# Kernel tuning notes

Hardware: AMD Instinct MI355X
Metric: run time of the kernel (lower is better)

Reference implementation:

```python
import jax, jax.numpy as jnp
import numpy as np

SXY_BF, SC_BF = 70.0, 12.0
COMPAT_BF, COMPAT_SPATIAL = 4.0, 2.0
SXY_SPATIAL = 6
NUM_ITER = 5
N_OUT = 21


def _gkern_depthwise(std, chans):
    # matches gkern(): sig_sq even -> r = sig_sq - 1, s = 2r+1
    sig_sq = std ** 2
    r = sig_sq if sig_sq % 2 else sig_sq - 1
    s = 2 * r + 1
    yy, xx = np.meshgrid(np.arange(s), np.arange(s), indexing='ij')
    k = np.exp(-(((yy - r) ** 2 + (xx - r) ** 2) / (2.0 * sig_sq)))
    k = k / k.sum()
    # original builds a [C,C,s,s] diagonal kernel == depthwise [C,1,s,s]
    return jnp.asarray(np.broadcast_to(k[None, None], (chans, 1, s, s)).copy(), jnp.float32)


def setup_inputs() -> dict:
    key = jax.random.key(0)
    k1, k2 = jax.random.split(key)
    unary = jax.random.uniform(k1, (2, N_OUT, 64, 64), dtype=jnp.float32)
    ref = jax.random.uniform(k2, (2, 3, 64, 64), dtype=jnp.float32) * 255.0  # RGB image
    gk = _gkern_depthwise(SXY_SPATIAL, N_OUT)
    kstd = jnp.asarray([SXY_BF, SXY_BF, SC_BF, SC_BF, SC_BF], jnp.float32)
    return {"unary": unary, "ref": ref, "gk": gk, "kstd": kstd}


def _crf_forward(unary, ref, gk, kstd):
    N, C, H, W = unary.shape
    P = H * W
    # stacked reference features: [y, x, r, g, b]
    yy, xx = jnp.meshgrid(jnp.arange(H, dtype=jnp.float32),
                          jnp.arange(W, dtype=jnp.float32), indexing='ij')
    grid = jnp.broadcast_to(jnp.stack([yy, xx])[None], (N, 2, H, W))
    stacked = jnp.concatenate([grid, ref], axis=1)  # [N,5,H,W]
    feats = (stacked / kstd[None, :, None, None]).reshape(N, -1, P).transpose(0, 2, 1)  # [N,P,5]
    # exact dense Gaussian (bilateral) kernel: K[p,q] = exp(-||f_p - f_q||^2 / 2)
    sq = jnp.sum(feats * feats, axis=-1)  # [N,P]
    d2 = sq[:, :, None] + sq[:, None, :] - 2.0 * jnp.einsum('npd,nqd->npq', feats, feats)
    K = jnp.exp(-0.5 * jnp.maximum(d2, 0.0))  # [N,P,P]

    U = jnp.log(jnp.clip(unary, 1e-5, 1.0))
    q = jax.nn.softmax(U, axis=1)
    pad = gk.shape[-1] // 2
    for i in range(NUM_ITER):
        qbf = jnp.einsum('npq,ncq->ncp', K, q.reshape(N, C, P)).reshape(N, C, H, W)
        qsf = jax.lax.conv_general_dilated(
            q, gk, window_strides=(1, 1), padding=[(pad, pad), (pad, pad)],
            feature_group_count=C, dimension_numbers=('NCHW', 'OIHW', 'NCHW'))
        q_hat = U + COMPAT_BF * qbf + COMPAT_SPATIAL * qsf
        q = jax.nn.softmax(q_hat, axis=1)  # normalize_final_iter=True
    return q


def reference(unary, ref, gk, kstd):
    return _crf_forward(unary, ref, gk, kstd)
```

## Files before the change

### kernel.cpp

```cpp
#include <hip/hip_runtime.h>
#include <math.h>

#ifndef __has_builtin
#define __has_builtin(x) 0
#endif
#if __has_builtin(__builtin_amdgcn_exp2f)
#define EXP2F(x) __builtin_amdgcn_exp2f(x)
#else
#define EXP2F(x) exp2f(x)
#endif

#define L2E  1.44269504088896340736f
#define RL2E 0.69314718055994530942f

#define NBATCH 2
#define NC 21
#define NP 4096
#define KR 35
#define KS 71

typedef _Float16 half_t;
typedef _Float16 h8 __attribute__((ext_vector_type(8)));
typedef _Float16 h4 __attribute__((ext_vector_type(4)));
typedef float f4 __attribute__((ext_vector_type(4)));
#define MFMA16(a, b, c) __builtin_amdgcn_mfma_f32_16x16x32_f16((a), (b), (c), 0, 0, 0)

#define PTILE 128
#define NPT   32
#define SQ    16
#define CHUNK 256
#define STEPS 8
#define NBBIL (NBATCH * NPT * SQ)
#define NBCONV (NBATCH * NC)
#define SEGS_PER_S 1024
#define SEG_HALVES 256

#define OFF_QFEAT 0
#define OFF_QSOA  65536
#define OFF_UT    114688
#define OFF_QSF   311296
#define OFF_G     483328
#define OFF_QH16  485376
#define OFF_PART  845824

#define LDS_BYTES 27648
#define QLS_STRIDE 264

__global__ __launch_bounds__(256) void setup_kernel(
    const float* __restrict__ unary, const float* __restrict__ ref,
    const float* __restrict__ kstd, float* __restrict__ ws,
    float* __restrict__ outq)
{
    int gid = blockIdx.x * 256 + threadIdx.x;
    if (gid < 4096) {
        float s = 0.f;
        for (int t = -KR; t <= KR; ++t) s += expf(-(float)(t * t) * (1.0f / 72.0f));
        int y = gid >> 6, yp = gid & 63;
        int d = y - yp;
        float v = (d >= -KR && d <= KR) ? expf(-(float)(d * d) * (1.0f / 72.0f)) / s : 0.f;
        ((half_t*)(ws + OFF_G))[gid] = (half_t)v;
    }
    if (gid >= NBATCH * NP) return;
    int n = gid >> 12, p = gid & (NP - 1);
    int y = p >> 6, x = p & 63;
    float k0 = kstd[0], k1 = kstd[1], k2 = kstd[2], k3 = kstd[3], k4 = kstd[4];
    const float* rp = ref + n * 3 * NP + p;
    float f0 = (float)y / k0;
    float f1 = (float)x / k1;
    float f2_ = rp[0]      / k2;
    float f3 = rp[NP]     / k3;
    float f4_ = rp[2 * NP] / k4;
    float sq = f0*f0 + f1*f1 + f2_*f2_ + f3*f3 + f4_*f4_;
    float h  = -0.5f * L2E * sq;
    float* qf = ws + OFF_QFEAT + gid * 8;
    qf[0]=L2E*f0; qf[1]=L2E*f1; qf[2]=L2E*f2_; qf[3]=L2E*f3; qf[4]=L2E*f4_;
    qf[5]=h; qf[6]=0.f; qf[7]=0.f;
    float* qs = ws + OFF_QSOA;
    qs[0*8192 + gid] = L2E*f0;  qs[1*8192 + gid] = L2E*f1;
    qs[2*8192 + gid] = L2E*f2_; qs[3*8192 + gid] = L2E*f3;
    qs[4*8192 + gid] = L2E*f4_; qs[5*8192 + gid] = h;

    float U[NC], e[NC];
    const float* up = unary + n * NC * NP + p;
    float m = -1e30f;
    for (int c = 0; c < NC; ++c) {
        float u = up[c * NP];
        u = fminf(fmaxf(u, 1e-5f), 1.0f);
        U[c] = logf(u);
        m = fmaxf(m, U[c]);
    }
    float ssum = 0.f;
    for (int c = 0; c < NC; ++c) { e[c] = EXP2F(L2E * (U[c] - m)); ssum += e[c]; }
    float inv = 1.0f / ssum;
    float* ut = ws + OFF_UT + gid * 24;
    half_t* qh = (half_t*)(ws + OFF_QH16);
    for (int c = 0; c < NC; ++c) {
        float qv = e[c] * inv;
        ut[c] = U[c];
        qh[(n * 24 + c) * NP + p] = (half_t)qv;
        outq[(n * NC + c) * NP + p] = qv;
    }
    ut[21] = 0.f; ut[22] = 0.f; ut[23] = 0.f;
    qh[(n * 24 + 21) * NP + p] = (half_t)0.f;
    qh[(n * 24 + 22) * NP + p] = (half_t)0.f;
    qh[(n * 24 + 23) * NP + p] = (half_t)0.f;
}

__global__ __launch_bounds__(256) void bilat_conv_kernel(
    const float* __restrict__ qfeatA,
    const float* __restrict__ qsoa,
    const half_t* __restrict__ qh16,
    const half_t* __restrict__ gmat,
    half_t* __restrict__ part,
    float* __restrict__ qsf)
{
    __shared__ __align__(16) char lds[LDS_BYTES];
    int b = blockIdx.x;
    int tid = threadIdx.x;
    int l = tid & 63, w = tid >> 6;

    if (b < NBBIL) {
        int n  = b & 1;
        int pt = (b >> 1) & (NPT - 1);
        int s  = b >> 6;
        float*  qsoaS = (float*)lds;
        half_t* qls   = (half_t*)(lds + 6144);

        for (int i = tid; i < 6 * (CHUNK / 4); i += 256) {
            int d = i >> 6, g = i & 63;
            *(f4*)(qsoaS + d * CHUNK + g * 4) =
                *(const f4*)(qsoa + (size_t)d * 8192 + n * NP + s * CHUNK + g * 4);
        }
        for (int i = tid; i < 21 * (CHUNK / 8); i += 256) {
            int c = i >> 5, g = i & 31;
            *(h8*)(qls + c * QLS_STRIDE + g * 8) =
                *(const h8*)(qh16 + (size_t)(n * 24 + c) * NP + s * CHUNK + g * 8);
        }
        for (int i = tid; i < 11 * 33; i += 256) {
            int c = 21 + i / 33, g = i % 33;
            *(h8*)(qls + c * QLS_STRIDE + g * 8) = (h8)(half_t)0.f;
        }
        float pf[2][5], ph[2];
        #pragma unroll
        for (int mt = 0; mt < 2; ++mt) {
            const float* fp = qfeatA + (size_t)(n * NP + pt * PTILE + (w * 2 + mt) * 16 + (l & 15)) * 8;
            #pragma unroll
            for (int i = 0; i < 5; ++i) pf[mt][i] = fp[i] * RL2E;
            ph[mt] = fp[5];
        }
        f4 acc[2][2];
        #pragma unroll
        for (int mt = 0; mt < 2; ++mt) { acc[mt][0] = (f4)0.f; acc[mt][1] = (f4)0.f; }
        int kq = (l >> 4) * 8;
        __syncthreads();

        for (int step = 0; step < STEPS; ++step) {
            int qbase = step * 32 + kq;
            h8 kv[2];
            #pragma unroll
            for (int hf = 0; hf < 2; ++hf) {
                f4 qf0 = *(const f4*)(qsoaS + 0 * CHUNK + qbase + hf * 4);
                f4 qf1 = *(const f4*)(qsoaS + 1 * CHUNK + qbase + hf * 4);
                f4 qf2 = *(const f4*)(qsoaS + 2 * CHUNK + qbase + hf * 4);
                f4 qf3 = *(const f4*)(qsoaS + 3 * CHUNK + qbase + hf * 4);
                f4 qf4 = *(const f4*)(qsoaS + 4 * CHUNK + qbase + hf * 4);
                f4 qf5 = *(const f4*)(qsoaS + 5 * CHUNK + qbase + hf * 4);
                #pragma unroll
                for (int j2 = 0; j2 < 4; ++j2) {
                    float q0 = qf0[j2], q1 = qf1[j2], q2 = qf2[j2];
                    float q3 = qf3[j2], q4 = qf4[j2], qh = qf5[j2];
                    #pragma unroll
                    for (int mt = 0; mt < 2; ++mt) {
                        float e = ph[mt] + qh;
                        e = fmaf(pf[mt][0], q0, e);
                        e = fmaf(pf[mt][1], q1, e);
                        e = fmaf(pf[mt][2], q2, e);
                        e = fmaf(pf[mt][3], q3, e);
                        e = fmaf(pf[mt][4], q4, e);
                        kv[mt][hf * 4 + j2] = (half_t)EXP2F(e);
                    }
                }
            }
            h8 bf0 = *(const h8*)(qls + (size_t)(l & 15) * QLS_STRIDE + qbase);
            h8 bf1 = *(const h8*)(qls + (size_t)(16 + (l & 15)) * QLS_STRIDE + qbase);
            #pragma unroll
            for (int mt = 0; mt < 2; ++mt) {
                acc[mt][0] = MFMA16(kv[mt], bf0, acc[mt][0]);
                acc[mt][1] = MFMA16(kv[mt], bf1, acc[mt][1]);
            }
        }
        #pragma unroll
        for (int mt = 0; mt < 2; ++mt) {
            #pragma unroll
            for (int cht = 0; cht < 2; ++cht) {
                int segFlat = ((((s * 2 + n) * NPT + pt) * 4 + w) * 2 + mt) * 2 + cht;
                h4 hv;
                hv[0] = (half_t)acc[mt][cht][0];
                hv[1] = (half_t)acc[mt][cht][1];
                hv[2] = (half_t)acc[mt][cht][2];
                hv[3] = (half_t)acc[mt][cht][3];
                *(h4*)(part + (size_t)segFlat * SEG_HALVES + l * 4) = hv;
            }
        }
    } else {
        int cb = b - NBBIL;
        int n = cb / NC, c = cb % NC;
        half_t* qt = (half_t*)lds;
        half_t* gl = (half_t*)(lds + 9216);
        half_t* dl = (half_t*)(lds + 18432);

        for (int i = tid; i < 512; i += 256) {
            int row = i >> 3, g = i & 7;
            *(h8*)(gl + row * 72 + g * 8) = *(const h8*)(gmat + row * 64 + g * 8);
        }
        const half_t* qsrc = qh16 + (size_t)(n * 24 + c) * NP;
        for (int i = tid; i < 512; i += 256) {
            int row = i >> 3, g = i & 7;
            h8 v = *(const h8*)(qsrc + row * 64 + g * 8);
            #pragma unroll
            for (int k = 0; k < 8; ++k) qt[(g * 8 + k) * 72 + row] = v[k];
        }
        __syncthreads();

        int m0 = w * 16;
        f4 acc1[4];
        #pragma unroll
        for (int nt = 0; nt < 4; ++nt) acc1[nt] = (f4)0.f;
        #pragma unroll
        for (int ks = 0; ks < 2; ++ks) {
            h8 af = *(const h8*)(gl + (size_t)(m0 + (l & 15)) * 72 + ks * 32 + (l >> 4) * 8);
            #pragma unroll
            for (int nt = 0; nt < 4; ++nt) {
                h8 bf = *(const h8*)(qt + (size_t)(nt * 16 + (l & 15)) * 72 + ks * 32 + (l >> 4) * 8);
                acc1[nt] = MFMA16(af, bf, acc1[nt]);
            }
        }
        #pragma unroll
        for (int nt = 0; nt < 4; ++nt)
            #pragma unroll
            for (int r = 0; r < 4; ++r)
                dl[(size_t)(m0 + (l >> 4) * 4 + r) * 72 + nt * 16 + (l & 15)] = (half_t)acc1[nt][r];
        __syncthreads();

        f4 acc2[4];
        #pragma unroll
        for (int nt = 0; nt < 4; ++nt) acc2[nt] = (f4)0.f;
        #pragma unroll
        for (int ks = 0; ks < 2; ++ks) {
            h8 af = *(const h8*)(dl + (size_t)(m0 + (l & 15)) * 72 + ks * 32 + (l >> 4) * 8);
            #pragma unroll
            for (int nt = 0; nt < 4; ++nt) {
                h8 bf = *(const h8*)(gl + (size_t)(nt * 16 + (l & 15)) * 72 + ks * 32 + (l >> 4) * 8);
                acc2[nt] = MFMA16(af, bf, acc2[nt]);
            }
        }
        float* dst = qsf + (size_t)(n * NC + c) * NP;
        #pragma unroll
        for (int nt = 0; nt < 4; ++nt)
            #pragma unroll
            for (int r = 0; r < 4; ++r)
                dst[(size_t)(m0 + (l >> 4) * 4 + r) * 64 + nt * 16 + (l & 15)] = acc2[nt][r];
    }
}

__global__ __launch_bounds__(256) void reduce_update_kernel(
    const half_t* __restrict__ part, const float* __restrict__ ut_,
    const float* __restrict__ qsf, float* __restrict__ outq,
    half_t* __restrict__ qh16)
{
    __shared__ float red[4096];
    int rb = blockIdx.x;
    int tid = threadIdx.x;
    int n = rb & 1, pt = rb >> 1;

    float acc[16];
    #pragma unroll
    for (int k = 0; k < 16; ++k) acc[k] = 0.f;
    for (int s = 0; s < SQ; ++s) {
        size_t base = (size_t)(((s * 2 + n) * NPT + pt) * 16) * SEG_HALVES;
        #pragma unroll
        for (int k = 0; k < 4; ++k) {
            h4 v = *(const h4*)(part + base + (size_t)(k * 256 + tid) * 4);
            acc[k*4+0] += (float)v[0]; acc[k*4+1] += (float)v[1];
            acc[k*4+2] += (float)v[2]; acc[k*4+3] += (float)v[3];
        }
    }
    #pragma unroll
    for (int k = 0; k < 4; ++k)
        *(f4*)(red + (k * 256 + tid) * 4) =
            (f4){acc[k*4+0], acc[k*4+1], acc[k*4+2], acc[k*4+3]};
    __syncthreads();

    if (tid < PTILE) {
        int pp = tid;
        int p = pt * PTILE + pp;
        int gid = n * NP + p;
        int mt_g = pp >> 4;
        int wv = mt_g >> 1, mtl = mt_g & 1;
        int mrow = pp & 15;
        int lg = mrow >> 2, reg = mrow & 3;
        int segL = wv * 4 + mtl * 2;

        float lg_[NC], e[NC];
        const float* ut = ut_ + (size_t)gid * 24;
        const float* qs = qsf + (size_t)n * NC * NP + p;
        float m = -1e30f;
        #pragma unroll
        for (int c = 0; c < NC; ++c) {
            int cht = c >> 4, chL = c & 15;
            float qb = red[(segL + cht) * 256 + (lg * 16 + chL) * 4 + reg];
            float li = ut[c] + 4.0f * qb + 2.0f * qs[c * NP];
            lg_[c] = li;
            m = fmaxf(m, li);
        }
        float ssum = 0.f;
        #pragma unroll
        for (int c = 0; c < NC; ++c) { e[c] = EXP2F(L2E * (lg_[c] - m)); ssum += e[c]; }
        float inv = 1.0f / ssum;
        #pragma unroll
        for (int c = 0; c < NC; ++c) {
            float qv = e[c] * inv;
            outq[(size_t)(n * NC + c) * NP + p] = qv;
            qh16[(size_t)(n * 24 + c) * NP + p] = (half_t)qv;
        }
    }
}

extern "C" void kernel_launch(void* const* d_in, const int* in_sizes, int n_in,
                              void* d_out, int out_size, void* d_ws, size_t ws_size,
                              hipStream_t stream)
{
    const float* unary = (const float*)d_in[0];
    const float* ref   = (const float*)d_in[1];
    const float* kstd  = (const float*)d_in[3];
    float* ws   = (float*)d_ws;
    float* outq = (float*)d_out;

    const float*  qfeatA = ws + OFF_QFEAT;
    const float*  qsoa   = ws + OFF_QSOA;
    float*        ut     = ws + OFF_UT;
    float*        qsf    = ws + OFF_QSF;
    const half_t* gmat   = (const half_t*)(ws + OFF_G);
    half_t*       qh16   = (half_t*)(ws + OFF_QH16);
    half_t*       part   = (half_t*)(ws + OFF_PART);

    setup_kernel<<<32, 256, 0, stream>>>(unary, ref, kstd, ws, outq);
    for (int it = 0; it < 5; ++it) {
        bilat_conv_kernel<<<NBBIL + NBCONV, 256, 0, stream>>>(
            qfeatA, qsoa, qh16, gmat, part, qsf);
        reduce_update_kernel<<<64, 256, 0, stream>>>(part, ut, qsf, outq, qh16);
    }
}
```

Measured before the change: 159.5 us.

## Precompute dense bilateral kernel once in fp16 and stream it through GEMM

Splits the fused on-the-fly kernel generation and MFMA into a one-time kgen_kernel, which writes the full 2x4096x4096 fp16 Gaussian matrix to workspace in MFMA tile layout. A gemm_conv kernel then reads those tiles each of the five iterations instead of recomputing the exps. The GEMM tile grows to 256 rows per block, and the reduce kernel is resized to match. This removes repeated exp work in exchange for streaming about 64 MB of K per iteration from HBM or cache, and it needs a much larger workspace.

```diff
diff --git a/kernel.cpp b/kernel.cpp
--- a/kernel.cpp
+++ b/kernel.cpp
@@ -25,15 +25,23 @@
 typedef float f4 __attribute__((ext_vector_type(4)));
 #define MFMA16(a, b, c) __builtin_amdgcn_mfma_f32_16x16x32_f16((a), (b), (c), 0, 0, 0)
 
-#define PTILE 128
-#define NPT   32
-#define SQ    16
-#define CHUNK 256
-#define STEPS 8
-#define NBBIL (NBATCH * NPT * SQ)
+#define KG_PTILE 128
+#define KG_NPT   32
+#define KG_SQ    16
+#define KG_CHUNK 256
+#define KG_STEPS 8
+#define NBKG (NBATCH * KG_NPT * KG_SQ)
+
+#define GM_PTILE 256
+#define GM_NPT   16
+#define GM_SQ    16
+#define GM_SLICE 256
+#define GM_STEPS 8
+#define NBGM (NBATCH * GM_NPT * GM_SQ)
 #define NBCONV (NBATCH * NC)
-#define SEGS_PER_S 1024
+
 #define SEG_HALVES 256
+#define PART_PER_NPT 8192
 
 #define OFF_QFEAT 0
 #define OFF_QSOA  65536
@@ -42,6 +50,7 @@
 #define OFF_G     483328
 #define OFF_QH16  485376
 #define OFF_PART  845824
+#define OFF_KF    2942976
 
 #define LDS_BYTES 27648
 #define QLS_STRIDE 264
@@ -106,9 +115,74 @@
     qh[(n * 24 + 23) * NP + p] = (half_t)0.f;
 }
 
-__global__ __launch_bounds__(256) void bilat_conv_kernel(
+__global__ __launch_bounds__(256) void kgen_kernel(
     const float* __restrict__ qfeatA,
     const float* __restrict__ qsoa,
+    half_t* __restrict__ kf)
+{
+    __shared__ __align__(16) float qsoaS[6 * KG_CHUNK];
+    int b = blockIdx.x;
+    int tid = threadIdx.x;
+    int l = tid & 63, w = tid >> 6;
+    int n  = b & 1;
+    int pt = (b >> 1) & (KG_NPT - 1);
+    int s  = b >> 6;
+
+    for (int i = tid; i < 6 * (KG_CHUNK / 4); i += 256) {
+        int d = i >> 6, g = i & 63;
+        *(f4*)(qsoaS + d * KG_CHUNK + g * 4) =
+            *(const f4*)(qsoa + (size_t)d * 8192 + n * NP + s * KG_CHUNK + g * 4);
+    }
+    float pf[2][5], ph[2];
+    #pragma unroll
+    for (int mt = 0; mt < 2; ++mt) {
+        const float* fp = qfeatA + (size_t)(n * NP + pt * KG_PTILE + (w * 2 + mt) * 16 + (l & 15)) * 8;
+        #pragma unroll
+        for (int i = 0; i < 5; ++i) pf[mt][i] = fp[i] * RL2E;
+        ph[mt] = fp[5];
+    }
+    int kq = (l >> 4) * 8;
+    __syncthreads();
+
+    for (int step = 0; step < KG_STEPS; ++step) {
+        int qbase = step * 32 + kq;
+        h8 kv[2];
+        #pragma unroll
+        for (int hf = 0; hf < 2; ++hf) {
+            f4 qf0 = *(const f4*)(qsoaS + 0 * KG_CHUNK + qbase + hf * 4);
+            f4 qf1 = *(const f4*)(qsoaS + 1 * KG_CHUNK + qbase + hf * 4);
+            f4 qf2 = *(const f4*)(qsoaS + 2 * KG_CHUNK + qbase + hf * 4);
+            f4 qf3 = *(const f4*)(qsoaS + 3 * KG_CHUNK + qbase + hf * 4);
+            f4 qf4 = *(const f4*)(qsoaS + 4 * KG_CHUNK + qbase + hf * 4);
+            f4 qf5 = *(const f4*)(qsoaS + 5 * KG_CHUNK + qbase + hf * 4);
+            #pragma unroll
+            for (int j2 = 0; j2 < 4; ++j2) {
+                float q0 = qf0[j2], q1 = qf1[j2], q2 = qf2[j2];
+                float q3 = qf3[j2], q4 = qf4[j2], qh = qf5[j2];
+                #pragma unroll
+                for (int mt = 0; mt < 2; ++mt) {
+                    float e = ph[mt] + qh;
+                    e = fmaf(pf[mt][0], q0, e);
+                    e = fmaf(pf[mt][1], q1, e);
+                    e = fmaf(pf[mt][2], q2, e);
+                    e = fmaf(pf[mt][3], q3, e);
+                    e = fmaf(pf[mt][4], q4, e);
+                    kv[mt][hf * 4 + j2] = (half_t)EXP2F(e);
+                }
+            }
+        }
+        int qstep = s * KG_STEPS + step;
+        #pragma unroll
+        for (int mt = 0; mt < 2; ++mt) {
+            int pt16 = pt * 8 + w * 2 + mt;
+            size_t tile = ((size_t)(n * 256 + pt16) * 128 + qstep) * 512;
+            *(h8*)(kf + tile + l * 8) = kv[mt];
+        }
+    }
+}
+
+__global__ __launch_bounds__(256) void gemm_conv_kernel(
+    const half_t* __restrict__ kf,
     const half_t* __restrict__ qh16,
     const half_t* __restrict__ gmat,
     half_t* __restrict__ part,
@@ -119,81 +193,51 @@
     int tid = threadIdx.x;
     int l = tid & 63, w = tid >> 6;
 
-    if (b < NBBIL) {
+    if (b < NBGM) {
         int n  = b & 1;
-        int pt = (b >> 1) & (NPT - 1);
-        int s  = b >> 6;
-        float*  qsoaS = (float*)lds;
-        half_t* qls   = (half_t*)(lds + 6144);
-
-        for (int i = tid; i < 6 * (CHUNK / 4); i += 256) {
-            int d = i >> 6, g = i & 63;
-            *(f4*)(qsoaS + d * CHUNK + g * 4) =
-                *(const f4*)(qsoa + (size_t)d * 8192 + n * NP + s * CHUNK + g * 4);
-        }
-        for (int i = tid; i < 21 * (CHUNK / 8); i += 256) {
+        int pt = (b >> 1) & (GM_NPT - 1);
+        int qs = b >> 5;
+        half_t* qls = (half_t*)lds;
+
+        for (int i = tid; i < 21 * (GM_SLICE / 8); i += 256) {
             int c = i >> 5, g = i & 31;
             *(h8*)(qls + c * QLS_STRIDE + g * 8) =
-                *(const h8*)(qh16 + (size_t)(n * 24 + c) * NP + s * CHUNK + g * 8);
+                *(const h8*)(qh16 + (size_t)(n * 24 + c) * NP + qs * GM_SLICE + g * 8);
         }
         for (int i = tid; i < 11 * 33; i += 256) {
             int c = 21 + i / 33, g = i % 33;
             *(h8*)(qls + c * QLS_STRIDE + g * 8) = (h8)(half_t)0.f;
         }
-        float pf[2][5], ph[2];
-        #pragma unroll
-        for (int mt = 0; mt < 2; ++mt) {
-            const float* fp = qfeatA + (size_t)(n * NP + pt * PTILE + (w * 2 + mt) * 16 + (l & 15)) * 8;
-            #pragma unroll
-            for (int i = 0; i < 5; ++i) pf[mt][i] = fp[i] * RL2E;
-            ph[mt] = fp[5];
-        }
-        f4 acc[2][2];
-        #pragma unroll
-        for (int mt = 0; mt < 2; ++mt) { acc[mt][0] = (f4)0.f; acc[mt][1] = (f4)0.f; }
+        f4 acc[4][2];
+        #pragma unroll
+        for (int mt = 0; mt < 4; ++mt) { acc[mt][0] = (f4)0.f; acc[mt][1] = (f4)0.f; }
         int kq = (l >> 4) * 8;
         __syncthreads();
 
-        for (int step = 0; step < STEPS; ++step) {
+        #pragma unroll 2
+        for (int step = 0; step < GM_STEPS; ++step) {
             int qbase = step * 32 + kq;
-            h8 kv[2];
-            #pragma unroll
-            for (int hf = 0; hf < 2; ++hf) {
-                f4 qf0 = *(const f4*)(qsoaS + 0 * CHUNK + qbase + hf * 4);
-                f4 qf1 = *(const f4*)(qsoaS + 1 * CHUNK + qbase + hf * 4);
-                f4 qf2 = *(const f4*)(qsoaS + 2 * CHUNK + qbase + hf * 4);
-                f4 qf3 = *(const f4*)(qsoaS + 3 * CHUNK + qbase + hf * 4);
-                f4 qf4 = *(const f4*)(qsoaS + 4 * CHUNK + qbase + hf * 4);
-                f4 qf5 = *(const f4*)(qsoaS + 5 * CHUNK + qbase + hf * 4);
-                #pragma unroll
-                for (int j2 = 0; j2 < 4; ++j2) {
-                    float q0 = qf0[j2], q1 = qf1[j2], q2 = qf2[j2];
-                    float q3 = qf3[j2], q4 = qf4[j2], qh = qf5[j2];
-                    #pragma unroll
-                    for (int mt = 0; mt < 2; ++mt) {
-                        float e = ph[mt] + qh;
-                        e = fmaf(pf[mt][0], q0, e);
-                        e = fmaf(pf[mt][1], q1, e);
-                        e = fmaf(pf[mt][2], q2, e);
-                        e = fmaf(pf[mt][3], q3, e);
-                        e = fmaf(pf[mt][4], q4, e);
-                        kv[mt][hf * 4 + j2] = (half_t)EXP2F(e);
-                    }
-                }
+            int qstep = qs * GM_STEPS + step;
+            h8 av[4];
+            #pragma unroll
+            for (int mt = 0; mt < 4; ++mt) {
+                int pt16 = pt * 16 + w * 4 + mt;
+                size_t tile = ((size_t)(n * 256 + pt16) * 128 + qstep) * 512;
+                av[mt] = *(const h8*)(kf + tile + l * 8);
             }
             h8 bf0 = *(const h8*)(qls + (size_t)(l & 15) * QLS_STRIDE + qbase);
             h8 bf1 = *(const h8*)(qls + (size_t)(16 + (l & 15)) * QLS_STRIDE + qbase);
             #pragma unroll
-            for (int mt = 0; mt < 2; ++mt) {
-                acc[mt][0] = MFMA16(kv[mt], bf0, acc[mt][0]);
-                acc[mt][1] = MFMA16(kv[mt], bf1, acc[mt][1]);
-            }
-        }
-        #pragma unroll
-        for (int mt = 0; mt < 2; ++mt) {
+            for (int mt = 0; mt < 4; ++mt) {
+                acc[mt][0] = MFMA16(av[mt], bf0, acc[mt][0]);
+                acc[mt][1] = MFMA16(av[mt], bf1, acc[mt][1]);
+            }
+        }
+        #pragma unroll
+        for (int mt = 0; mt < 4; ++mt) {
             #pragma unroll
             for (int cht = 0; cht < 2; ++cht) {
-                int segFlat = ((((s * 2 + n) * NPT + pt) * 4 + w) * 2 + mt) * 2 + cht;
+                int segFlat = ((((qs * 2 + n) * GM_NPT + pt) * 16 + (w * 4 + mt)) * 2 + cht);
                 h4 hv;
                 hv[0] = (half_t)acc[mt][cht][0];
                 hv[1] = (half_t)acc[mt][cht][1];
@@ -203,7 +247,7 @@
             }
         }
     } else {
-        int cb = b - NBBIL;
+        int cb = b - NBGM;
         int n = cb / NC, c = cb % NC;
         half_t* qt = (half_t*)lds;
         half_t* gl = (half_t*)(lds + 9216);
@@ -268,38 +312,37 @@
     const float* __restrict__ qsf, float* __restrict__ outq,
     half_t* __restrict__ qh16)
 {
-    __shared__ float red[4096];
+    __shared__ float red[PART_PER_NPT];
     int rb = blockIdx.x;
     int tid = threadIdx.x;
     int n = rb & 1, pt = rb >> 1;
 
-    float acc[16];
+    float acc[32];
     #pragma unroll
-    for (int k = 0; k < 16; ++k) acc[k] = 0.f;
-    for (int s = 0; s < SQ; ++s) {
-        size_t base = (size_t)(((s * 2 + n) * NPT + pt) * 16) * SEG_HALVES;
-        #pragma unroll
-        for (int k = 0; k < 4; ++k) {
+    for (int k = 0; k < 32; ++k) acc[k] = 0.f;
+    for (int s = 0; s < GM_SQ; ++s) {
+        size_t base = (size_t)((s * 2 + n) * GM_NPT + pt) * PART_PER_NPT;
+        #pragma unroll
+        for (int k = 0; k < 8; ++k) {
             h4 v = *(const h4*)(part + base + (size_t)(k * 256 + tid) * 4);
             acc[k*4+0] += (float)v[0]; acc[k*4+1] += (float)v[1];
             acc[k*4+2] += (float)v[2]; acc[k*4+3] += (float)v[3];
         }
     }
     #pragma unroll
-    for (int k = 0; k < 4; ++k)
+    for (int k = 0; k < 8; ++k)
         *(f4*)(red + (k * 256 + tid) * 4) =
             (f4){acc[k*4+0], acc[k*4+1], acc[k*4+2], acc[k*4+3]};
     __syncthreads();
 
-    if (tid < PTILE) {
+    {
         int pp = tid;
-        int p = pt * PTILE + pp;
+        int p = pt * GM_PTILE + pp;
         int gid = n * NP + p;
         int mt_g = pp >> 4;
-        int wv = mt_g >> 1, mtl = mt_g & 1;
         int mrow = pp & 15;
         int lg = mrow >> 2, reg = mrow & 3;
-        int segL = wv * 4 + mtl * 2;
+        int segL = mt_g * 2;
 
         float lg_[NC], e[NC];
         const float* ut = ut_ + (size_t)gid * 24;
@@ -343,11 +386,13 @@
     const half_t* gmat   = (const half_t*)(ws + OFF_G);
     half_t*       qh16   = (half_t*)(ws + OFF_QH16);
     half_t*       part   = (half_t*)(ws + OFF_PART);
+    half_t*       kf     = (half_t*)(ws + OFF_KF);
 
     setup_kernel<<<32, 256, 0, stream>>>(unary, ref, kstd, ws, outq);
+    kgen_kernel<<<NBKG, 256, 0, stream>>>(qfeatA, qsoa, kf);
     for (int it = 0; it < 5; ++it) {
-        bilat_conv_kernel<<<NBBIL + NBCONV, 256, 0, stream>>>(
-            qfeatA, qsoa, qh16, gmat, part, qsf);
-        reduce_update_kernel<<<64, 256, 0, stream>>>(part, ut, qsf, outq, qh16);
-    }
-}
+        gemm_conv_kernel<<<NBGM + NBCONV, 256, 0, stream>>>(
+            kf, qh16, gmat, part, qsf);
+        reduce_update_kernel<<<32, 256, 0, stream>>>(part, ut, qsf, outq, qh16);
+    }
+}
```

Result: slower. 201.3 us (+26.2%).

## Double bilateral P-tile to 256 rows per block for more reuse of q-chunk

Applied to the files above, without the earlier changes.

Each bilateral block now handles 256 output pixels (4 m-tiles per wave) instead of 128, halving the number of P-tiles. Loaded q-feature and q-probability LDS data are reused across more MFMAs, and the LDS loads are hoisted ahead of the exp computation. The reduce kernel is adjusted to 32 blocks with all 256 threads doing the softmax update. The trade-off is fewer blocks (fewer waves to fill the GPU) and higher register pressure per thread.

```diff
diff --git a/kernel.cpp b/kernel.cpp
--- a/kernel.cpp
+++ b/kernel.cpp
@@ -25,15 +25,16 @@
 typedef float f4 __attribute__((ext_vector_type(4)));
 #define MFMA16(a, b, c) __builtin_amdgcn_mfma_f32_16x16x32_f16((a), (b), (c), 0, 0, 0)
 
-#define PTILE 128
-#define NPT   32
+#define PTILE 256
+#define NPT   16
 #define SQ    16
 #define CHUNK 256
 #define STEPS 8
 #define NBBIL (NBATCH * NPT * SQ)
 #define NBCONV (NBATCH * NC)
-#define SEGS_PER_S 1024
+
 #define SEG_HALVES 256
+#define PART_PER_NPT 8192
 
 #define OFF_QFEAT 0
 #define OFF_QSOA  65536
@@ -122,55 +123,57 @@
     if (b < NBBIL) {
         int n  = b & 1;
         int pt = (b >> 1) & (NPT - 1);
-        int s  = b >> 6;
+        int qs = b >> 5;
         float*  qsoaS = (float*)lds;
         half_t* qls   = (half_t*)(lds + 6144);
 
         for (int i = tid; i < 6 * (CHUNK / 4); i += 256) {
             int d = i >> 6, g = i & 63;
             *(f4*)(qsoaS + d * CHUNK + g * 4) =
-                *(const f4*)(qsoa + (size_t)d * 8192 + n * NP + s * CHUNK + g * 4);
+                *(const f4*)(qsoa + (size_t)d * 8192 + n * NP + qs * CHUNK + g * 4);
         }
         for (int i = tid; i < 21 * (CHUNK / 8); i += 256) {
             int c = i >> 5, g = i & 31;
             *(h8*)(qls + c * QLS_STRIDE + g * 8) =
-                *(const h8*)(qh16 + (size_t)(n * 24 + c) * NP + s * CHUNK + g * 8);
+                *(const h8*)(qh16 + (size_t)(n * 24 + c) * NP + qs * CHUNK + g * 8);
         }
         for (int i = tid; i < 11 * 33; i += 256) {
             int c = 21 + i / 33, g = i % 33;
             *(h8*)(qls + c * QLS_STRIDE + g * 8) = (h8)(half_t)0.f;
         }
-        float pf[2][5], ph[2];
-        #pragma unroll
-        for (int mt = 0; mt < 2; ++mt) {
-            const float* fp = qfeatA + (size_t)(n * NP + pt * PTILE + (w * 2 + mt) * 16 + (l & 15)) * 8;
+        float pf[4][5], ph[4];
+        #pragma unroll
+        for (int mt = 0; mt < 4; ++mt) {
+            const float* fp = qfeatA + (size_t)(n * NP + pt * PTILE + (w * 4 + mt) * 16 + (l & 15)) * 8;
             #pragma unroll
             for (int i = 0; i < 5; ++i) pf[mt][i] = fp[i] * RL2E;
             ph[mt] = fp[5];
         }
-        f4 acc[2][2];
-        #pragma unroll
-        for (int mt = 0; mt < 2; ++mt) { acc[mt][0] = (f4)0.f; acc[mt][1] = (f4)0.f; }
+        f4 acc[4][2];
+        #pragma unroll
+        for (int mt = 0; mt < 4; ++mt) { acc[mt][0] = (f4)0.f; acc[mt][1] = (f4)0.f; }
         int kq = (l >> 4) * 8;
         __syncthreads();
 
         for (int step = 0; step < STEPS; ++step) {
             int qbase = step * 32 + kq;
-            h8 kv[2];
+            f4 qd[6][2];
+            #pragma unroll
+            for (int d = 0; d < 6; ++d) {
+                qd[d][0] = *(const f4*)(qsoaS + d * CHUNK + qbase);
+                qd[d][1] = *(const f4*)(qsoaS + d * CHUNK + qbase + 4);
+            }
+            h8 bf0 = *(const h8*)(qls + (size_t)(l & 15) * QLS_STRIDE + qbase);
+            h8 bf1 = *(const h8*)(qls + (size_t)(16 + (l & 15)) * QLS_STRIDE + qbase);
+            h8 kv[4];
             #pragma unroll
             for (int hf = 0; hf < 2; ++hf) {
-                f4 qf0 = *(const f4*)(qsoaS + 0 * CHUNK + qbase + hf * 4);
-                f4 qf1 = *(const f4*)(qsoaS + 1 * CHUNK + qbase + hf * 4);
-                f4 qf2 = *(const f4*)(qsoaS + 2 * CHUNK + qbase + hf * 4);
-                f4 qf3 = *(const f4*)(qsoaS + 3 * CHUNK + qbase + hf * 4);
-                f4 qf4 = *(const f4*)(qsoaS + 4 * CHUNK + qbase + hf * 4);
-                f4 qf5 = *(const f4*)(qsoaS + 5 * CHUNK + qbase + hf * 4);
                 #pragma unroll
                 for (int j2 = 0; j2 < 4; ++j2) {
-                    float q0 = qf0[j2], q1 = qf1[j2], q2 = qf2[j2];
-                    float q3 = qf3[j2], q4 = qf4[j2], qh = qf5[j2];
+                    float q0 = qd[0][hf][j2], q1 = qd[1][hf][j2], q2 = qd[2][hf][j2];
+                    float q3 = qd[3][hf][j2], q4 = qd[4][hf][j2], qh = qd[5][hf][j2];
                     #pragma unroll
-                    for (int mt = 0; mt < 2; ++mt) {
+                    for (int mt = 0; mt < 4; ++mt) {
                         float e = ph[mt] + qh;
                         e = fmaf(pf[mt][0], q0, e);
                         e = fmaf(pf[mt][1], q1, e);
@@ -181,19 +184,17 @@
                     }
                 }
             }
-            h8 bf0 = *(const h8*)(qls + (size_t)(l & 15) * QLS_STRIDE + qbase);
-            h8 bf1 = *(const h8*)(qls + (size_t)(16 + (l & 15)) * QLS_STRIDE + qbase);
-            #pragma unroll
-            for (int mt = 0; mt < 2; ++mt) {
+            #pragma unroll
+            for (int mt = 0; mt < 4; ++mt) {
                 acc[mt][0] = MFMA16(kv[mt], bf0, acc[mt][0]);
                 acc[mt][1] = MFMA16(kv[mt], bf1, acc[mt][1]);
             }
         }
         #pragma unroll
-        for (int mt = 0; mt < 2; ++mt) {
+        for (int mt = 0; mt < 4; ++mt) {
             #pragma unroll
             for (int cht = 0; cht < 2; ++cht) {
-                int segFlat = ((((s * 2 + n) * NPT + pt) * 4 + w) * 2 + mt) * 2 + cht;
+                int segFlat = ((((qs * 2 + n) * NPT + pt) * 16 + (w * 4 + mt)) * 2 + cht);
                 h4 hv;
                 hv[0] = (half_t)acc[mt][cht][0];
                 hv[1] = (half_t)acc[mt][cht][1];
@@ -268,48 +269,47 @@
     const float* __restrict__ qsf, float* __restrict__ outq,
     half_t* __restrict__ qh16)
 {
-    __shared__ float red[4096];
+    __shared__ float red[PART_PER_NPT];
     int rb = blockIdx.x;
     int tid = threadIdx.x;
     int n = rb & 1, pt = rb >> 1;
 
-    float acc[16];
+    float acc[32];
     #pragma unroll
-    for (int k = 0; k < 16; ++k) acc[k] = 0.f;
+    for (int k = 0; k < 32; ++k) acc[k] = 0.f;
     for (int s = 0; s < SQ; ++s) {
-        size_t base = (size_t)(((s * 2 + n) * NPT + pt) * 16) * SEG_HALVES;
-        #pragma unroll
-        for (int k = 0; k < 4; ++k) {
+        size_t base = (size_t)((s * 2 + n) * NPT + pt) * PART_PER_NPT;
+        #pragma unroll
+        for (int k = 0; k < 8; ++k) {
             h4 v = *(const h4*)(part + base + (size_t)(k * 256 + tid) * 4);
             acc[k*4+0] += (float)v[0]; acc[k*4+1] += (float)v[1];
             acc[k*4+2] += (float)v[2]; acc[k*4+3] += (float)v[3];
         }
     }
     #pragma unroll
-    for (int k = 0; k < 4; ++k)
+    for (int k = 0; k < 8; ++k)
         *(f4*)(red + (k * 256 + tid) * 4) =
             (f4){acc[k*4+0], acc[k*4+1], acc[k*4+2], acc[k*4+3]};
     __syncthreads();
 
-    if (tid < PTILE) {
+    {
         int pp = tid;
         int p = pt * PTILE + pp;
         int gid = n * NP + p;
         int mt_g = pp >> 4;
-        int wv = mt_g >> 1, mtl = mt_g & 1;
         int mrow = pp & 15;
         int lg = mrow >> 2, reg = mrow & 3;
-        int segL = wv * 4 + mtl * 2;
+        int segL = mt_g * 2;
 
         float lg_[NC], e[NC];
         const float* ut = ut_ + (size_t)gid * 24;
-        const float* qs = qsf + (size_t)n * NC * NP + p;
+        const float* qsp = qsf + (size_t)n * NC * NP + p;
         float m = -1e30f;
         #pragma unroll
         for (int c = 0; c < NC; ++c) {
             int cht = c >> 4, chL = c & 15;
             float qb = red[(segL + cht) * 256 + (lg * 16 + chL) * 4 + reg];
-            float li = ut[c] + 4.0f * qb + 2.0f * qs[c * NP];
+            float li = ut[c] + 4.0f * qb + 2.0f * qsp[c * NP];
             lg_[c] = li;
             m = fmaxf(m, li);
         }
@@ -348,6 +348,6 @@
     for (int it = 0; it < 5; ++it) {
         bilat_conv_kernel<<<NBBIL + NBCONV, 256, 0, stream>>>(
             qfeatA, qsoa, qh16, gmat, part, qsf);
-        reduce_update_kernel<<<64, 256, 0, stream>>>(part, ut, qsf, outq, qh16);
+        reduce_update_kernel<<<32, 256, 0, stream>>>(part, ut, qsf, outq, qh16);
     }
 }
```

New measurement: 172.5 us. 8.1% more time.
